# Performance work log

Hardware: AMD Instinct MI355X
Metric: run time of the kernel (lower is better)

Reference implementation:

```python
import jax, jax.numpy as jnp
import numpy as np

N_NODES = 50000


def gcn_layer(x, src, dst, ew, W, b, n_nodes):
    # PyG GCNConv: add self-loops (weight 1), symmetric deg^-1/2 normalization,
    # linear transform, scatter-add aggregation at destination, then bias.
    loop = jnp.arange(n_nodes, dtype=src.dtype)
    s = jnp.concatenate([src, loop])
    d = jnp.concatenate([dst, loop])
    w = jnp.concatenate([ew, jnp.ones((n_nodes,), dtype=ew.dtype)])
    deg = jax.ops.segment_sum(w, d, num_segments=n_nodes)  # [N]
    dinv = jnp.where(deg > 0, jax.lax.rsqrt(jnp.where(deg > 0, deg, 1.0)), 0.0)
    norm = dinv[s] * w * dinv[d]  # [E+N]
    h = x @ W  # [N, out]
    msg = h[s] * norm[:, None]  # gather + scale, [E+N, out]
    out = jax.ops.segment_sum(msg, d, num_segments=n_nodes)  # scatter-add
    return out + b


def setup_inputs() -> dict:
    key = jax.random.key(0)
    k1, k2, k3, k4, k5, k6, k7 = jax.random.split(key, 7)
    N, E, C_IN, C_OUT = N_NODES, 600000, 128, 128
    x = jax.random.normal(k1, (N, C_IN), dtype=jnp.float32)
    edge_index = jax.random.randint(k2, (2, E), 0, N, dtype=jnp.int64)
    edge_weight = jax.random.uniform(k3, (E,), dtype=jnp.float32)
    # Glorot-style init like PyG's Linear default
    s1 = 1.0 / np.sqrt(C_IN)
    s2 = 1.0 / np.sqrt(C_OUT)
    W1 = jax.random.uniform(k4, (C_IN, C_OUT), jnp.float32, -s1, s1)
    b1 = jnp.zeros((C_OUT,), dtype=jnp.float32)
    W2 = jax.random.uniform(k5, (C_OUT, C_OUT), jnp.float32, -s2, s2)
    b2 = jnp.zeros((C_OUT,), dtype=jnp.float32)
    return {"x": x, "edge_index": edge_index, "edge_weight": edge_weight,
            "W1": W1, "b1": b1, "W2": W2, "b2": b2}


def reference(x, edge_index, edge_weight, W1, b1, W2, b2):
    src, dst = edge_index[0], edge_index[1]
    h = jax.nn.relu(gcn_layer(x, src, dst, edge_weight, W1, b1, N_NODES))
    return jax.nn.relu(gcn_layer(h, src, dst, edge_weight, W2, b2, N_NODES))
```

## Files before the change

### kernel.cpp

```cpp
#include <hip/hip_runtime.h>
#include <math.h>

#define CH   128
#define CH4  32
#define TPB  256
#define SCANB 1024
#define WIMG 16384
#define NREP 8
#define FIXS 1048576.0f

typedef __attribute__((ext_vector_type(8))) short short8;
typedef __attribute__((ext_vector_type(4))) float floatx4;
typedef __attribute__((ext_vector_type(8))) float float8;
typedef unsigned long long u64;

static __device__ __forceinline__ unsigned short f2bf(float f) {
    unsigned u = __float_as_uint(f);
    return (unsigned short)((u + 0x7fffu + ((u >> 16) & 1u)) >> 16);
}
static __device__ __forceinline__ float bf2f(unsigned short s) {
    return __uint_as_float(((unsigned)s) << 16);
}
static __device__ __forceinline__ float8 bf8_to_f8(short8 u) {
    float8 f;
    #pragma unroll
    for (int i = 0; i < 8; ++i) f[i] = bf2f((unsigned short)u[i]);
    return f;
}

__global__ void k_prep(const float* __restrict__ W1, const float* __restrict__ W2,
                       short* __restrict__ Wsplit, float4* __restrict__ zbase,
                       int nzero4, int nbPrep) {
    int bx = blockIdx.x;
    if (bx >= nbPrep) {
        int i = (bx - nbPrep) * TPB + threadIdx.x;
        if (i < nzero4) zbase[i] = make_float4(0.f, 0.f, 0.f, 0.f);
        return;
    }
    int i = bx * TPB + threadIdx.x;
    if (i >= 2 * CH * CH) return;
    int layer = i >> 14;
    int idx   = i & 16383;
    int k = idx >> 7, c = idx & 127;
    float w = (layer ? W2 : W1)[k * CH + c];
    unsigned short hi = f2bf(w);
    unsigned short lo = f2bf(w - bf2f(hi));
    int colh = c >> 6, nn = c & 63;
    int kt = k >> 5, q = (k & 31) >> 3, j = k & 7;
    int ns = nn >> 4, ln = q * 16 + (nn & 15);
    size_t base = (size_t)(layer * 2 + colh) * WIMG;
    size_t off  = ((size_t)(kt * 4 + ns) * 64 + ln) * 8 + j;
    Wsplit[base + off]        = (short)hi;
    Wsplit[base + 8192 + off] = (short)lo;
}

static __device__ __forceinline__ void gemm_body_f32(
        const float* __restrict__ X, const short* __restrict__ Wfrag,
        unsigned short* __restrict__ H, int n, int tile, int colh, int tid) {
    __shared__ __align__(16) short sW[2][4][4][64][8];
    {
        const float4* gsrc = (const float4*)Wfrag;
        float4* ldst = (float4*)sW;
        #pragma unroll
        for (int i = 0; i < 8; ++i)
            ldst[i * TPB + tid] = gsrc[i * TPB + tid];
    }
    __syncthreads();

    const int lane = tid & 63;
    const int wv   = tid >> 6;
    const int q    = lane >> 4;
    const int m    = lane & 15;
    const int row0 = tile * 64 + wv * 16;
    if (row0 >= n) return;

    int rrow = row0 + m;
    if (rrow > n - 1) rrow = n - 1;

    const float4* xr = (const float4*)(X + (size_t)rrow * CH);
    float4 xa[4][2];
    #pragma unroll
    for (int kt = 0; kt < 4; ++kt) {
        xa[kt][0] = xr[kt * 8 + q * 2 + 0];
        xa[kt][1] = xr[kt * 8 + q * 2 + 1];
    }

    floatx4 acc[4];
    #pragma unroll
    for (int ns = 0; ns < 4; ++ns) acc[ns] = (floatx4){0.f, 0.f, 0.f, 0.f};

    #pragma unroll
    for (int kt = 0; kt < 4; ++kt) {
        float xf[8] = { xa[kt][0].x, xa[kt][0].y, xa[kt][0].z, xa[kt][0].w,
                        xa[kt][1].x, xa[kt][1].y, xa[kt][1].z, xa[kt][1].w };
        short8 ah, al;
        #pragma unroll
        for (int j = 0; j < 8; ++j) {
            float v = xf[j];
            unsigned short h = f2bf(v);
            ah[j] = (short)h;
            al[j] = (short)f2bf(v - bf2f(h));
        }
        #pragma unroll
        for (int ns = 0; ns < 4; ++ns) {
            short8 bh = *(const short8*)&sW[0][kt][ns][lane][0];
            short8 bl = *(const short8*)&sW[1][kt][ns][lane][0];
            acc[ns] = __builtin_amdgcn_mfma_f32_16x16x32_bf16(ah, bh, acc[ns], 0, 0, 0);
            acc[ns] = __builtin_amdgcn_mfma_f32_16x16x32_bf16(al, bh, acc[ns], 0, 0, 0);
            acc[ns] = __builtin_amdgcn_mfma_f32_16x16x32_bf16(ah, bl, acc[ns], 0, 0, 0);
        }
    }

    #pragma unroll
    for (int ns = 0; ns < 4; ++ns) {
        #pragma unroll
        for (int reg = 0; reg < 4; ++reg) {
            int r = row0 + q * 4 + reg;
            if (r < n)
                H[(size_t)r * CH + colh * 64 + ns * 16 + m] = f2bf(acc[ns][reg]);
        }
    }
}

__global__ __launch_bounds__(TPB, 4)
void k_gemm_rank(const float* __restrict__ X, const short* __restrict__ Wsplit,
                 unsigned short* __restrict__ H, int n,
                 const int* __restrict__ dst, const float* __restrict__ ew,
                 u64* __restrict__ counts_rep, int* __restrict__ rank,
                 int E, int nbE4, int Np) {
    int bx = blockIdx.x;
    if (bx < nbE4) {
        int stride = nbE4 * TPB;
        int e = bx * TPB + threadIdx.x;
        #pragma unroll
        for (int it = 0; it < 4; ++it, e += stride) {
            if (e < E) {
                int d = dst[e];
                if ((unsigned)d < (unsigned)n) {
                    int rep = e & (NREP - 1);
                    u64 pk = (1ull << 40) |
                             (u64)(unsigned)__float2uint_rn(ew[e] * FIXS);
                    u64 old = atomicAdd(&counts_rep[(size_t)rep * Np + d], pk);
                    rank[e] = (int)(old >> 40);
                }
            }
        }
    } else {
        bx -= nbE4;
        int colh = bx & 1;
        gemm_body_f32(X, Wsplit + (size_t)colh * WIMG, H, n, bx >> 1, colh,
                      threadIdx.x);
    }
}

__global__ __launch_bounds__(SCANB)
void k_scan1(const u64* __restrict__ counts_rep, int Np,
             int* __restrict__ counts_tot, int* __restrict__ repoff8,
             int* __restrict__ row_start, float* __restrict__ dinv,
             int* __restrict__ partials, int* __restrict__ pp_s,
             int* __restrict__ done, int nb, int n) {
    __shared__ int s[SCANB];
    __shared__ int slast;
    int gid = blockIdx.x * SCANB + threadIdx.x;
    int c[NREP];
    int v = 0;
    u64 wsum = 0;
    #pragma unroll
    for (int r = 0; r < NREP; ++r) {
        u64 pk = (gid < n) ? counts_rep[(size_t)r * Np + gid] : 0ull;
        c[r] = (int)(pk >> 40);
        wsum += pk & ((1ull << 40) - 1);
        v += c[r];
    }
    s[threadIdx.x] = v;
    __syncthreads();
    for (int off = 1; off < SCANB; off <<= 1) {
        int t = (threadIdx.x >= off) ? s[threadIdx.x - off] : 0;
        __syncthreads();
        s[threadIdx.x] += t;
        __syncthreads();
    }
    if (gid < n) {
        row_start[gid]  = s[threadIdx.x] - v;
        counts_tot[gid] = v;
        dinv[gid] = rsqrtf(1.0f + (float)wsum * (1.0f / FIXS));
        int pre = 0;
        int ro[NREP];
        #pragma unroll
        for (int r = 0; r < NREP; ++r) { ro[r] = pre; pre += c[r]; }
        ((int4*)repoff8)[gid * 2 + 0] = make_int4(ro[0], ro[1], ro[2], ro[3]);
        ((int4*)repoff8)[gid * 2 + 1] = make_int4(ro[4], ro[5], ro[6], ro[7]);
    }
    if (threadIdx.x == SCANB - 1) {
        partials[blockIdx.x] = s[SCANB - 1];
        __threadfence();
        int old = atomicAdd(done, 1);
        slast = (old == nb - 1);
    }
    __syncthreads();
    if (slast && threadIdx.x < 64) {
        int pv = (threadIdx.x < nb) ? atomicAdd(&partials[threadIdx.x], 0) : 0;
        int inc = pv;
        #pragma unroll
        for (int off = 1; off < 64; off <<= 1) {
            int t = __shfl_up(inc, off, 64);
            if ((threadIdx.x & 63) >= off) inc += t;
        }
        if (threadIdx.x < nb) pp_s[threadIdx.x] = inc - pv;
    }
}

__global__ void k_fill(const int* __restrict__ src, const int* __restrict__ dst,
                       const float* __restrict__ ew, const int* __restrict__ row_start,
                       const int* __restrict__ pp_s, const int* __restrict__ repoff8,
                       const int* __restrict__ rank, const float* __restrict__ dinv,
                       int2* __restrict__ edges, int E, int n) {
    int e = blockIdx.x * blockDim.x + threadIdx.x;
    if (e >= E) return;
    int s = src[e], d = dst[e];
    if ((unsigned)s >= (unsigned)n || (unsigned)d >= (unsigned)n) return;
    int rep = e & (NREP - 1);
    int base = row_start[d] + pp_s[d >> 10] + repoff8[d * NREP + rep];
    edges[base + rank[e]] = make_int2(s, __float_as_int(ew[e] * dinv[s]));
}

static __device__ __forceinline__ float8 agg_node8(
        const short8* __restrict__ h8, const int2* __restrict__ edges,
        float di, const float8 b, int node, int tx,
        const int* __restrict__ row_start, const int* __restrict__ pp_s,
        const int* __restrict__ counts) {
    float8 hv = bf8_to_f8(h8[(size_t)node * 16 + tx]);
    float8 acc;
    #pragma unroll
    for (int i = 0; i < 8; ++i) acc[i] = 0.f;

    int j   = row_start[node] + pp_s[node >> 10];
    int end = j + counts[node];

    for (; j + 8 <= end; j += 8) {
        int2 e[8];
        #pragma unroll
        for (int i = 0; i < 8; ++i) e[i] = edges[j + i];
        short8 g[8];
        #pragma unroll
        for (int i = 0; i < 8; ++i) g[i] = h8[(size_t)e[i].x * 16 + tx];
        #pragma unroll
        for (int i = 0; i < 8; ++i) {
            float w = __int_as_float(e[i].y);
            float8 gf = bf8_to_f8(g[i]);
            #pragma unroll
            for (int c = 0; c < 8; ++c) acc[c] += gf[c] * w;
        }
    }
    if (j + 4 <= end) {
        int2 e[4];
        #pragma unroll
        for (int i = 0; i < 4; ++i) e[i] = edges[j + i];
        short8 g[4];
        #pragma unroll
        for (int i = 0; i < 4; ++i) g[i] = h8[(size_t)e[i].x * 16 + tx];
        #pragma unroll
        for (int i = 0; i < 4; ++i) {
            float w = __int_as_float(e[i].y);
            float8 gf = bf8_to_f8(g[i]);
            #pragma unroll
            for (int c = 0; c < 8; ++c) acc[c] += gf[c] * w;
        }
        j += 4;
    }
    for (; j < end; ++j) {
        int2 e0 = edges[j];
        float w0 = __int_as_float(e0.y);
        float8 gf = bf8_to_f8(h8[(size_t)e0.x * 16 + tx]);
        #pragma unroll
        for (int c = 0; c < 8; ++c) acc[c] += gf[c] * w0;
    }

    float di2 = di * di;
    float8 o;
    #pragma unroll
    for (int c = 0; c < 8; ++c) o[c] = di2 * hv[c] + di * acc[c] + b[c];
    return o;
}

__global__ __launch_bounds__(TPB)
void k_agg_gemm(const unsigned short* __restrict__ h,
                const int* __restrict__ row_start, const int* __restrict__ pp_s,
                const int* __restrict__ counts, const int2* __restrict__ edges,
                const float* __restrict__ dinv, const float* __restrict__ bias,
                const short* __restrict__ W2img,
                unsigned short* __restrict__ h2, int n) {
    __shared__ __align__(16) short8 tile[16 * 17];
    const int tid = threadIdx.x;

    const int bnode0 = (int)blockIdx.x * 16;
    const int tx = tid & 15;
    const int tg = tid >> 4;
    const int node = bnode0 + tg;
    float8 b;
    #pragma unroll
    for (int c = 0; c < 8; ++c) b[c] = bias[tx * 8 + c];
    short8 u;
    if (node < n) {
        float8 o = agg_node8((const short8*)h, edges, dinv[node], b, node,
                             tx, row_start, pp_s, counts);
        #pragma unroll
        for (int c = 0; c < 8; ++c) u[c] = (short)f2bf(fmaxf(o[c], 0.f));
    } else {
        #pragma unroll
        for (int c = 0; c < 8; ++c) u[c] = 0;
    }
    tile[tg * 17 + tx] = u;
    __syncthreads();

    const int lane = tid & 63;
    const int wv   = tid >> 6;
    const int q    = lane >> 4;
    const int m    = lane & 15;
    const int ch   = wv & 1;
    const int ns0  = (wv >> 1) * 2;

    short8 a[4];
    #pragma unroll
    for (int kt = 0; kt < 4; ++kt)
        a[kt] = tile[m * 17 + kt * 4 + q];

    const short8* w2f = (const short8*)(W2img + (size_t)ch * WIMG);

    floatx4 acc[2];
    #pragma unroll
    for (int i = 0; i < 2; ++i) acc[i] = (floatx4){0.f, 0.f, 0.f, 0.f};

    #pragma unroll
    for (int kt = 0; kt < 4; ++kt) {
        #pragma unroll
        for (int i = 0; i < 2; ++i) {
            short8 bh = w2f[(kt * 4 + ns0 + i) * 64 + lane];
            acc[i] = __builtin_amdgcn_mfma_f32_16x16x32_bf16(a[kt], bh, acc[i],
                                                             0, 0, 0);
        }
    }

    #pragma unroll
    for (int i = 0; i < 2; ++i)
        #pragma unroll
        for (int reg = 0; reg < 4; ++reg) {
            int r = bnode0 + q * 4 + reg;
            if (r < n)
                h2[(size_t)r * CH + ch * 64 + (ns0 + i) * 16 + m] =
                    f2bf(acc[i][reg]);
        }
}

__global__ __launch_bounds__(TPB)
void k_aggregate2(const unsigned short* __restrict__ h,
                  const int* __restrict__ row_start, const int* __restrict__ pp_s,
                  const int* __restrict__ counts, const int2* __restrict__ edges,
                  const float* __restrict__ dinv, const float* __restrict__ bias,
                  float* __restrict__ out, int n) {
    int t = blockIdx.x * blockDim.x + threadIdx.x;
    int node = t >> 4;
    if (node >= n) return;
    int tx = t & 15;
    float8 b;
    #pragma unroll
    for (int c = 0; c < 8; ++c) b[c] = bias[tx * 8 + c];
    float8 o = agg_node8((const short8*)h, edges, dinv[node], b, node, tx,
                         row_start, pp_s, counts);
    float4 lo = make_float4(fmaxf(o[0], 0.f), fmaxf(o[1], 0.f),
                            fmaxf(o[2], 0.f), fmaxf(o[3], 0.f));
    float4 hi = make_float4(fmaxf(o[4], 0.f), fmaxf(o[5], 0.f),
                            fmaxf(o[6], 0.f), fmaxf(o[7], 0.f));
    ((float4*)out)[(size_t)node * CH4 + tx * 2 + 0] = lo;
    ((float4*)out)[(size_t)node * CH4 + tx * 2 + 1] = hi;
}

extern "C" void kernel_launch(void* const* d_in, const int* in_sizes, int n_in,
                              void* d_out, int out_size, void* d_ws, size_t ws_size,
                              hipStream_t stream) {
    const float* x  = (const float*)d_in[0];
    const int*   ei = (const int*)d_in[1];
    const float* ew = (const float*)d_in[2];
    const float* W1 = (const float*)d_in[3];
    const float* b1 = (const float*)d_in[4];
    const float* W2 = (const float*)d_in[5];
    const float* b2 = (const float*)d_in[6];
    float* out = (float*)d_out;

    const int N = in_sizes[0] / CH;
    const int E = in_sizes[2];
    const int* src = ei;
    const int* dst = ei + E;

    size_t Np = ((size_t)N + 255) & ~(size_t)255;
    size_t Ep = ((size_t)E + 63) & ~(size_t)63;
    float* ws          = (float*)d_ws;
    float* dinv        = ws;
    unsigned short* h  = (unsigned short*)(dinv + Np);
    unsigned short* h2 = h + (size_t)N * CH;
    u64*   counts_rep  = (u64*)(h2 + (size_t)N * CH);
    int*   done        = (int*)(counts_rep + NREP * Np);
    int    nzero4      = (int)((2 * NREP * Np + 64) / 4);
    int*  counts_tot   = done + 64;
    int*  row_start    = counts_tot + Np;
    int*  repoff8      = row_start + Np;
    int*  rank         = repoff8 + NREP * Np;
    int*  partials     = rank + Ep;
    int*  pp_s         = partials + 64;
    int2* edges        = (int2*)(pp_s + 64);
    short* Wsplit      = (short*)(edges + E);

    const int nbE    = (E + TPB - 1) / TPB;
    const int nbE4   = (E + TPB * 4 - 1) / (TPB * 4);
    const int nbAgg  = (int)(((size_t)N * 16 + TPB - 1) / TPB);
    const int nbScan = (N + SCANB - 1) / SCANB;
    const int nbGemm = 2 * ((N + 63) / 64);
    const int nbAG   = (N + 15) / 16;
    const int nbPrep = (2 * CH * CH + TPB - 1) / TPB;
    const int nbZero = (nzero4 + TPB - 1) / TPB;

    k_prep     <<<nbPrep + nbZero, TPB, 0, stream>>>(W1, W2, Wsplit,
                                                     (float4*)counts_rep,
                                                     nzero4, nbPrep);

    k_gemm_rank<<<nbE4 + nbGemm, TPB, 0, stream>>>(x, Wsplit, h, N, dst, ew,
                                                   counts_rep, rank, E, nbE4,
                                                   (int)Np);
    k_scan1    <<<nbScan, SCANB, 0, stream>>>(counts_rep, (int)Np, counts_tot,
                                              repoff8, row_start, dinv,
                                              partials, pp_s, done, nbScan, N);
    k_fill     <<<nbE, TPB, 0, stream>>>(src, dst, ew, row_start, pp_s, repoff8,
                                         rank, dinv, edges, E, N);

    k_agg_gemm <<<nbAG, TPB, 0, stream>>>(h, row_start, pp_s, counts_tot,
                                          edges, dinv, b1,
                                          Wsplit + 2 * (size_t)WIMG, h2, N);
    k_aggregate2<<<nbAgg, TPB, 0, stream>>>(h2, row_start, pp_s, counts_tot,
                                            edges, dinv, b2, out, N);
}
```

Baseline: 206.2 us.

## Halve atomic replicas, use wave-shuffle block scan, prefetch edges in aggregation

```diff
diff --git a/kernel.cpp b/kernel.cpp
--- a/kernel.cpp
+++ b/kernel.cpp
@@ -6,7 +6,7 @@
 #define TPB  256
 #define SCANB 1024
 #define WIMG 16384
-#define NREP 8
+#define NREP 4
 #define FIXS 1048576.0f
 
 typedef __attribute__((ext_vector_type(8))) short short8;
@@ -155,13 +155,17 @@
 
 __global__ __launch_bounds__(SCANB)
 void k_scan1(const u64* __restrict__ counts_rep, int Np,
-             int* __restrict__ counts_tot, int* __restrict__ repoff8,
+             int* __restrict__ counts_tot, int* __restrict__ repoff,
              int* __restrict__ row_start, float* __restrict__ dinv,
              int* __restrict__ partials, int* __restrict__ pp_s,
              int* __restrict__ done, int nb, int n) {
-    __shared__ int s[SCANB];
-    __shared__ int slast;
-    int gid = blockIdx.x * SCANB + threadIdx.x;
+    __shared__ int swt[SCANB / 64];
+    __shared__ int slastS;
+    const int tid  = threadIdx.x;
+    const int lane = tid & 63;
+    const int wid  = tid >> 6;
+    const int gid  = blockIdx.x * SCANB + tid;
+
     int c[NREP];
     int v = 0;
     u64 wsum = 0;
@@ -172,47 +176,59 @@
         wsum += pk & ((1ull << 40) - 1);
         v += c[r];
     }
-    s[threadIdx.x] = v;
+    int inc = v;
+    #pragma unroll
+    for (int off = 1; off < 64; off <<= 1) {
+        int t = __shfl_up(inc, off, 64);
+        if (lane >= off) inc += t;
+    }
+    if (lane == 63) swt[wid] = inc;
     __syncthreads();
-    for (int off = 1; off < SCANB; off <<= 1) {
-        int t = (threadIdx.x >= off) ? s[threadIdx.x - off] : 0;
-        __syncthreads();
-        s[threadIdx.x] += t;
-        __syncthreads();
-    }
+    if (wid == 0) {
+        int wv_ = (lane < SCANB / 64) ? swt[lane] : 0;
+        int winc = wv_;
+        #pragma unroll
+        for (int off = 1; off < SCANB / 64; off <<= 1) {
+            int t = __shfl_up(winc, off, 64);
+            if (lane >= off) winc += t;
+        }
+        if (lane < SCANB / 64) swt[lane] = winc - wv_;
+    }
+    __syncthreads();
+    const int myincl = inc + swt[wid];
+
     if (gid < n) {
-        row_start[gid]  = s[threadIdx.x] - v;
+        row_start[gid]  = myincl - v;
         counts_tot[gid] = v;
         dinv[gid] = rsqrtf(1.0f + (float)wsum * (1.0f / FIXS));
         int pre = 0;
         int ro[NREP];
         #pragma unroll
         for (int r = 0; r < NREP; ++r) { ro[r] = pre; pre += c[r]; }
-        ((int4*)repoff8)[gid * 2 + 0] = make_int4(ro[0], ro[1], ro[2], ro[3]);
-        ((int4*)repoff8)[gid * 2 + 1] = make_int4(ro[4], ro[5], ro[6], ro[7]);
-    }
-    if (threadIdx.x == SCANB - 1) {
-        partials[blockIdx.x] = s[SCANB - 1];
+        ((int4*)repoff)[gid] = make_int4(ro[0], ro[1], ro[2], ro[3]);
+    }
+    if (tid == SCANB - 1) {
+        partials[blockIdx.x] = myincl;
         __threadfence();
         int old = atomicAdd(done, 1);
-        slast = (old == nb - 1);
+        slastS = (old == nb - 1);
     }
     __syncthreads();
-    if (slast && threadIdx.x < 64) {
-        int pv = (threadIdx.x < nb) ? atomicAdd(&partials[threadIdx.x], 0) : 0;
-        int inc = pv;
+    if (slastS && tid < 64) {
+        int pv = (tid < nb) ? atomicAdd(&partials[tid], 0) : 0;
+        int i2 = pv;
         #pragma unroll
         for (int off = 1; off < 64; off <<= 1) {
-            int t = __shfl_up(inc, off, 64);
-            if ((threadIdx.x & 63) >= off) inc += t;
-        }
-        if (threadIdx.x < nb) pp_s[threadIdx.x] = inc - pv;
+            int t = __shfl_up(i2, off, 64);
+            if ((tid & 63) >= off) i2 += t;
+        }
+        if (tid < nb) pp_s[tid] = i2 - pv;
     }
 }
 
 __global__ void k_fill(const int* __restrict__ src, const int* __restrict__ dst,
                        const float* __restrict__ ew, const int* __restrict__ row_start,
-                       const int* __restrict__ pp_s, const int* __restrict__ repoff8,
+                       const int* __restrict__ pp_s, const int* __restrict__ repoff,
                        const int* __restrict__ rank, const float* __restrict__ dinv,
                        int2* __restrict__ edges, int E, int n) {
     int e = blockIdx.x * blockDim.x + threadIdx.x;
@@ -220,7 +236,7 @@
     int s = src[e], d = dst[e];
     if ((unsigned)s >= (unsigned)n || (unsigned)d >= (unsigned)n) return;
     int rep = e & (NREP - 1);
-    int base = row_start[d] + pp_s[d >> 10] + repoff8[d * NREP + rep];
+    int base = row_start[d] + pp_s[d >> 10] + repoff[d * NREP + rep];
     edges[base + rank[e]] = make_int2(s, __float_as_int(ew[e] * dinv[s]));
 }
 
@@ -237,13 +253,22 @@
     int j   = row_start[node] + pp_s[node >> 10];
     int end = j + counts[node];
 
-    for (; j + 8 <= end; j += 8) {
-        int2 e[8];
+    int2 e[8];
+    bool have = (j + 8 <= end);
+    if (have) {
         #pragma unroll
         for (int i = 0; i < 8; ++i) e[i] = edges[j + i];
+    }
+    while (have) {
         short8 g[8];
         #pragma unroll
         for (int i = 0; i < 8; ++i) g[i] = h8[(size_t)e[i].x * 16 + tx];
+        int2 en[8];
+        const bool haven = (j + 16 <= end);
+        if (haven) {
+            #pragma unroll
+            for (int i = 0; i < 8; ++i) en[i] = edges[j + 8 + i];
+        }
         #pragma unroll
         for (int i = 0; i < 8; ++i) {
             float w = __int_as_float(e[i].y);
@@ -251,17 +276,21 @@
             #pragma unroll
             for (int c = 0; c < 8; ++c) acc[c] += gf[c] * w;
         }
+        j += 8;
+        have = haven;
+        #pragma unroll
+        for (int i = 0; i < 8; ++i) e[i] = en[i];
     }
     if (j + 4 <= end) {
-        int2 e[4];
-        #pragma unroll
-        for (int i = 0; i < 4; ++i) e[i] = edges[j + i];
+        int2 e4[4];
+        #pragma unroll
+        for (int i = 0; i < 4; ++i) e4[i] = edges[j + i];
         short8 g[4];
         #pragma unroll
-        for (int i = 0; i < 4; ++i) g[i] = h8[(size_t)e[i].x * 16 + tx];
+        for (int i = 0; i < 4; ++i) g[i] = h8[(size_t)e4[i].x * 16 + tx];
         #pragma unroll
         for (int i = 0; i < 4; ++i) {
-            float w = __int_as_float(e[i].y);
+            float w = __int_as_float(e4[i].y);
             float8 gf = bf8_to_f8(g[i]);
             #pragma unroll
             for (int c = 0; c < 8; ++c) acc[c] += gf[c] * w;
@@ -403,8 +432,8 @@
     int    nzero4      = (int)((2 * NREP * Np + 64) / 4);
     int*  counts_tot   = done + 64;
     int*  row_start    = counts_tot + Np;
-    int*  repoff8      = row_start + Np;
-    int*  rank         = repoff8 + NREP * Np;
+    int*  repoff       = row_start + Np;
+    int*  rank         = repoff + NREP * Np;
     int*  partials     = rank + Ep;
     int*  pp_s         = partials + 64;
     int2* edges        = (int2*)(pp_s + 64);
@@ -427,9 +456,9 @@
                                                    counts_rep, rank, E, nbE4,
                                                    (int)Np);
     k_scan1    <<<nbScan, SCANB, 0, stream>>>(counts_rep, (int)Np, counts_tot,
-                                              repoff8, row_start, dinv,
+                                              repoff, row_start, dinv,
                                               partials, pp_s, done, nbScan, N);
-    k_fill     <<<nbE, TPB, 0, stream>>>(src, dst, ew, row_start, pp_s, repoff8,
+    k_fill     <<<nbE, TPB, 0, stream>>>(src, dst, ew, row_start, pp_s, repoff,
                                          rank, dinv, edges, E, N);
 
     k_agg_gemm <<<nbAG, TPB, 0, stream>>>(h, row_start, pp_s, counts_tot,
```

Result: no change. 210.1 us (+1.9%).
